# Kernel tuning notes

Hardware: AMD Instinct MI355X
Metric: run time of the kernel (lower is better)

Reference implementation:

```python
import jax, jax.numpy as jnp
import numpy as np

B, A_IN, C_IN, H, W_ = 8, 16, 4, 64, 64   # batch, input atoms, input capsules, spatial
K, C_OUT, A_OUT, ROUTINGS = 5, 8, 32, 3
EPS = 1e-7


def setup_inputs() -> dict:
    key = jax.random.key(0)
    k1, k2 = jax.random.split(key)
    x = jax.random.normal(k1, (B, A_IN, C_IN, H, W_), dtype=jnp.float32)
    # kaiming_uniform_(fan_in, relu): bound = sqrt(3) * sqrt(2) / sqrt(fan_in)
    fan_in = A_IN * K * K
    bound = float(np.sqrt(6.0 / fan_in))
    W = jax.random.uniform(k2, (C_OUT * A_OUT, A_IN, K, K), jnp.float32, -bound, bound)
    b = jnp.full((1, 1, C_OUT, A_OUT), 0.1, dtype=jnp.float32)
    return {"x": x, "W": W, "b": b}


def _squash(v):
    # v: (..., atoms); SegCaps squash with epsilon inside sqrt
    sq = jnp.sum(v * v, axis=-1, keepdims=True)
    return v * (sq / (1.0 + sq) / jnp.sqrt(sq + EPS))


def reference(x, W, b):
    # Faithful to torch: permute then raw row-major reshapes (byte reinterpret)
    t = jnp.transpose(x, (2, 0, 3, 4, 1))                      # (C_IN, B, H, W, A_IN)
    t = t.reshape(C_IN * B, H, W_, A_IN).reshape(-1, A_IN, H, W_)
    conv = jax.lax.conv_general_dilated(
        t, W, window_strides=(1, 1), padding="SAME",
        dimension_numbers=("NCHW", "OIHW", "NCHW"))             # (C_IN*B, C_OUT*A_OUT, h, w)
    ch, cw = conv.shape[2], conv.shape[3]
    votes = conv.reshape(B, C_IN, ch, cw, C_OUT, A_OUT)         # raw reinterpret, as in torch
    biases = jnp.tile(b, (ch, cw, 1, 1))                        # (h, w, C_OUT, A_OUT)

    # dynamic routing (SegCaps update_routing)
    logits = jnp.zeros((B, C_IN, ch, cw, C_OUT), dtype=votes.dtype)
    activation = None
    for _ in range(ROUTINGS):
        route = jax.nn.softmax(logits, axis=-1)                 # (B, Cin, h, w, Cout)
        preact = jnp.einsum("bihwo,bihwoa->bhwoa", route, votes) + biases
        activation = _squash(preact)                            # (B, h, w, Cout, A)
        agreement = jnp.einsum("bihwoa,bhwoa->bihwo", votes, activation)
        logits = logits + agreement
    return jnp.transpose(activation, (0, 4, 3, 1, 2))           # (B, A_OUT, C_OUT, h, w)
```

## Files before the change

kernel.cpp:

```cpp
#include <hip/hip_runtime.h>
#include <hip/hip_bf16.h>


typedef _Float16 half8 __attribute__((ext_vector_type(8)));
typedef _Float16 half4v __attribute__((ext_vector_type(4)));
typedef float floatx4 __attribute__((ext_vector_type(4)));

#define EPSF 1e-7f

__global__ __launch_bounds__(256) void k_prep(const float* __restrict__ x,
                                              const float* __restrict__ W,
                                              _Float16* __restrict__ th,
                                              _Float16* __restrict__ Wp) {
  const int tid = threadIdx.x;
  if (blockIdx.x < 256) {
    __shared__ float lin[32 * 306 + 18];
    const int bid = blockIdx.x;
    const int n   = bid >> 3;
    const int a0h = (bid >> 2) & 1;
    const int W0  = (bid & 3) * 16;
    const int ci = n >> 3, b0 = n & 7;
    const float* xb = x + b0 * 262144 + ci * 4096 + W0;
    for (int p = 0; p < 8; ++p) {
      int rr = p * 64 + (tid >> 2);
      int qq = (tid & 3) * 4;
      int a1 = rr >> 5, m = rr & 31;
      float4 v = *(const float4*)(xb + a1 * 16384 + (a0h * 32 + m) * 64 + qq);
      float* d = lin + m * 306 + a1 * 18 + qq;
      d[0] = v.x; d[1] = v.y; d[2] = v.z; d[3] = v.w;
    }
    __syncthreads();
    _Float16* tb = th + (size_t)n * 65536 + a0h * 32768 + W0 * 128;
    for (int hh = 0; hh < 4; ++hh) {
      int w1 = tid >> 4, a1 = tid & 15;
      half8 v;
#pragma unroll
      for (int j = 0; j < 8; ++j)
        v[j] = (_Float16)lin[(j * 4 + hh) * 306 + a1 * 18 + w1];
      *(half8*)(tb + hh * 8192 + w1 * 128 + a1 * 8) = v;
    }
  } else {
    int id = (blockIdx.x - 256) * 256 + tid;
    int a  = id & 15;
    int oc = (id >> 4) & 255;
    int kk = id >> 12;
    Wp[id] = (kk < 25) ? (_Float16)W[oc * 400 + a * 25 + kk] : (_Float16)0.0f;
  }
}

__global__ __launch_bounds__(256, 3) void k_conv(
    const _Float16* __restrict__ th, const _Float16* __restrict__ Wp,
    _Float16* __restrict__ votes) {
  __shared__ _Float16 slab[5440];
  const int y = blockIdx.x;
  const int n = blockIdx.y;
  const int tid = threadIdx.x;

  for (int c = tid; c < 680; c += 256) {
    int ah  = c / 340;
    int rem = c - ah * 340;
    int rr  = rem / 68;
    int cc  = rem - rr * 68;
    int row = y + rr - 2;
    int col = cc - 2;
    half8 v = {};
    if (row >= 0 && row < 64 && col >= 0 && col < 64)
      v = *(const half8*)(th + (size_t)(((n * 2 + ah) * 64 + row) * 64 + col) * 8);
    *(half8*)(slab + c * 8) = v;
  }

  const int lane  = tid & 63;
  const int wv    = tid >> 6;
  const int col16 = lane & 15;
  const int quad  = lane >> 4;
  const int t     = quad >> 1;
  const int a0h   = quad & 1;
  const int m0    = wv * 64;

  floatx4 acc[4][4] = {};

  const _Float16* wb = Wp + (size_t)t * 4096 + (m0 + col16) * 16 + a0h * 8;
  half8 af[4], a1[4], a2[4], bf[4], b1[4];
#pragma unroll
  for (int oct = 0; oct < 4; ++oct) {
    af[oct] = *(const half8*)(wb + oct * 256);
    a1[oct] = *(const half8*)(wb + 8192 + oct * 256);
  }

  __syncthreads();

  {
    int kkb = t;
    int ky = kkb / 5, kx = kkb - ky * 5;
    const _Float16* lb = slab + (a0h * 340 + ky * 68 + col16 + kx) * 8;
#pragma unroll
    for (int xt = 0; xt < 4; ++xt)
      bf[xt] = *(const half8*)(lb + xt * 128);
  }

  for (int s = 0; s < 13; ++s) {
    int s2 = (s + 2 < 13) ? s + 2 : 12;
#pragma unroll
    for (int oct = 0; oct < 4; ++oct)
      a2[oct] = *(const half8*)(wb + (size_t)s2 * 8192 + oct * 256);
    int kkb1 = 2 * (s + 1) + t; if (kkb1 > 24) kkb1 = 24;
    int ky1 = kkb1 / 5, kx1 = kkb1 - ky1 * 5;
    const _Float16* lb1 = slab + (a0h * 340 + ky1 * 68 + col16 + kx1) * 8;
#pragma unroll
    for (int xt = 0; xt < 4; ++xt)
      b1[xt] = *(const half8*)(lb1 + xt * 128);
#pragma unroll
    for (int oct = 0; oct < 4; ++oct)
#pragma unroll
      for (int xt = 0; xt < 4; ++xt)
        acc[oct][xt] = __builtin_amdgcn_mfma_f32_16x16x32_f16(
            af[oct], bf[xt], acc[oct][xt], 0, 0, 0);
#pragma unroll
    for (int oct = 0; oct < 4; ++oct) { af[oct] = a1[oct]; a1[oct] = a2[oct]; }
#pragma unroll
    for (int xt = 0; xt < 4; ++xt) bf[xt] = b1[xt];
  }

  _Float16* vbase = votes + (size_t)n * 1048576 + y * 64;
#pragma unroll
  for (int oct = 0; oct < 4; ++oct)
#pragma unroll
    for (int xt = 0; xt < 4; ++xt)
#pragma unroll
      for (int r = 0; r < 4; ++r) {
        int oc = m0 + oct * 16 + quad * 4 + r;
        int xx = xt * 16 + col16;
        vbase[(size_t)oc * 4096 + xx] = (_Float16)acc[oct][xt][r];
      }
}

__global__ __launch_bounds__(256) void k_routing3(
    const _Float16* __restrict__ votes, const float* __restrict__ bias,
    float* __restrict__ out) {
  __shared__ float so[128 * 37];
  const int tid  = threadIdx.x;
  const int lane = tid & 63;
  const int wv   = tid >> 6;
  const int bid  = blockIdx.x;
  const int bv = bid >> 7;
  const int h  = (bid >> 1) & 63;
  const int W0 = (bid & 1) * 32;

  float4 bia = *(const float4*)(bias + lane * 4);
  const int o = lane >> 3;
  const int m = lane & 7;

  float act[8][4];

  const _Float16* vb0 = votes + (size_t)bv * 4194304 + h * 16384
                        + (W0 + wv * 8) * 256 + lane * 4;
  half4v vn[4];
#pragma unroll
  for (int i = 0; i < 4; ++i)
    vn[i] = *(const half4v*)(vb0 + (size_t)i * 1048576);

  for (int k = 0; k < 8; ++k) {
    float4 v[4];
#pragma unroll
    for (int i = 0; i < 4; ++i)
      v[i] = make_float4((float)vn[i].x, (float)vn[i].y,
                         (float)vn[i].z, (float)vn[i].w);
    if (k < 7) {
#pragma unroll
      for (int i = 0; i < 4; ++i)
        vn[i] = *(const half4v*)(vb0 + (k + 1) * 256 + (size_t)i * 1048576);
    }

    float logit[4] = {0.f, 0.f, 0.f, 0.f};
#pragma unroll
    for (int r = 0; r < 3; ++r) {
      float route[4];
#pragma unroll
      for (int i = 0; i < 4; ++i) {
        float mx = logit[i];
        mx = fmaxf(mx, __shfl_xor(mx, 8, 64));
        mx = fmaxf(mx, __shfl_xor(mx, 16, 64));
        mx = fmaxf(mx, __shfl_xor(mx, 32, 64));
        float e = __expf(logit[i] - mx);
        float s = e;
        s += __shfl_xor(s, 8, 64);
        s += __shfl_xor(s, 16, 64);
        s += __shfl_xor(s, 32, 64);
        route[i] = e / s;
      }
      float pr[4] = {bia.x, bia.y, bia.z, bia.w};
#pragma unroll
      for (int i = 0; i < 4; ++i) {
        pr[0] = fmaf(route[i], v[i].x, pr[0]);
        pr[1] = fmaf(route[i], v[i].y, pr[1]);
        pr[2] = fmaf(route[i], v[i].z, pr[2]);
        pr[3] = fmaf(route[i], v[i].w, pr[3]);
      }
      float sq = pr[0]*pr[0] + pr[1]*pr[1] + pr[2]*pr[2] + pr[3]*pr[3];
      sq += __shfl_xor(sq, 1, 64);
      sq += __shfl_xor(sq, 2, 64);
      sq += __shfl_xor(sq, 4, 64);
      float scale = sq / (1.f + sq) / sqrtf(sq + EPSF);
#pragma unroll
      for (int j = 0; j < 4; ++j) act[k][j] = pr[j] * scale;

      if (r < 2) {
#pragma unroll
        for (int i = 0; i < 4; ++i) {
          float ag = v[i].x*act[k][0] + v[i].y*act[k][1]
                   + v[i].z*act[k][2] + v[i].w*act[k][3];
          ag += __shfl_xor(ag, 1, 64);
          ag += __shfl_xor(ag, 2, 64);
          ag += __shfl_xor(ag, 4, 64);
          logit[i] += ag;
        }
      }
    }
  }

  float* ob = out + (size_t)bv * 1048576 + h * 64 + W0;
#pragma unroll
  for (int ph = 0; ph < 2; ++ph) {
    if (ph) __syncthreads();
#pragma unroll
    for (int k = 0; k < 8; ++k)
#pragma unroll
      for (int jj = 0; jj < 2; ++jj) {
        int rc = m * 16 + jj * 8 + o;
        so[rc * 37 + wv * 8 + k] = act[k][2 * ph + jj];
      }
    __syncthreads();
    for (int p = 0; p < 4; ++p) {
      int rc = p * 32 + (tid >> 3);
      int mm = rc >> 4, jj = (rc >> 3) & 1, oo = rc & 7;
      int rg = mm * 32 + (2 * ph + jj) * 8 + oo;
      int w0 = (tid & 7) * 4;
      const float* sp = so + rc * 37 + w0;
      float4 val = make_float4(sp[0], sp[1], sp[2], sp[3]);
      *(float4*)(ob + (size_t)rg * 4096 + w0) = val;
    }
  }
}

extern "C" void kernel_launch(void* const* d_in, const int* in_sizes, int n_in,
                              void* d_out, int out_size, void* d_ws, size_t ws_size,
                              hipStream_t stream) {
  const float* x  = (const float*)d_in[0];
  const float* W  = (const float*)d_in[1];
  const float* b  = (const float*)d_in[2];
  float* out = (float*)d_out;

  _Float16* th    = (_Float16*)d_ws;
  _Float16* Wp    = th + 2097152;
  _Float16* votes = Wp + 106496;

  k_prep<<<672, 256, 0, stream>>>(x, W, th, Wp);
  k_conv<<<dim3(64, 32), 256, 0, stream>>>(th, Wp, votes);
  k_routing3<<<1024, 256, 0, stream>>>(votes, b, out);
}
```

Baseline: 152.8 us.

## Pre-pad conv input, swap MFMA operands for vector stores, simplify routing

The prep kernel now writes the transposed fp16 input into a zero-padded 68x68 buffer, cleared by a memset, so the conv slab load needs no bounds checks. The conv kernel swaps MFMA operand order so each lane holds four consecutive x outputs, which allows half4 vector stores of votes. It also drops the occupancy hint from launch_bounds. The routing kernel specialises the first iteration to uniform routes of 1/8, drops the softmax max-subtraction, and halves the pixels per block, doubling the grid. The memset adds an extra launch, and dropping the max-subtraction relies on logits staying small.

```diff
diff --git a/kernel.cpp b/kernel.cpp
--- a/kernel.cpp
+++ b/kernel.cpp
@@ -8,9 +8,10 @@
 
 #define EPSF 1e-7f
 
+
 __global__ __launch_bounds__(256) void k_prep(const float* __restrict__ x,
                                               const float* __restrict__ W,
-                                              _Float16* __restrict__ th,
+                                              _Float16* __restrict__ thp,
                                               _Float16* __restrict__ Wp) {
   const int tid = threadIdx.x;
   if (blockIdx.x < 256) {
@@ -30,14 +31,16 @@
       d[0] = v.x; d[1] = v.y; d[2] = v.z; d[3] = v.w;
     }
     __syncthreads();
-    _Float16* tb = th + (size_t)n * 65536 + a0h * 32768 + W0 * 128;
     for (int hh = 0; hh < 4; ++hh) {
       int w1 = tid >> 4, a1 = tid & 15;
+      int h = hh * 16 + ((W0 + w1) >> 2);
+      int w = ((W0 + w1) & 3) * 16 + a1;
       half8 v;
 #pragma unroll
       for (int j = 0; j < 8; ++j)
         v[j] = (_Float16)lin[(j * 4 + hh) * 306 + a1 * 18 + w1];
-      *(half8*)(tb + hh * 8192 + w1 * 128 + a1 * 8) = v;
+      size_t chunk = ((size_t)(n * 2 + a0h) * 68 + (h + 2)) * 68 + (w + 2);
+      *(half8*)(thp + chunk * 8) = v;
     }
   } else {
     int id = (blockIdx.x - 256) * 256 + tid;
@@ -48,25 +51,20 @@
   }
 }
 
-__global__ __launch_bounds__(256, 3) void k_conv(
-    const _Float16* __restrict__ th, const _Float16* __restrict__ Wp,
+__global__ __launch_bounds__(256) void k_conv(
+    const _Float16* __restrict__ thp, const _Float16* __restrict__ Wp,
     _Float16* __restrict__ votes) {
   __shared__ _Float16 slab[5440];
   const int y = blockIdx.x;
   const int n = blockIdx.y;
   const int tid = threadIdx.x;
 
+  const size_t base0 = (size_t)(n * 2) * 36992 + (size_t)y * 544;
   for (int c = tid; c < 680; c += 256) {
-    int ah  = c / 340;
+    int ah  = (c >= 340);
     int rem = c - ah * 340;
-    int rr  = rem / 68;
-    int cc  = rem - rr * 68;
-    int row = y + rr - 2;
-    int col = cc - 2;
-    half8 v = {};
-    if (row >= 0 && row < 64 && col >= 0 && col < 64)
-      v = *(const half8*)(th + (size_t)(((n * 2 + ah) * 64 + row) * 64 + col) * 8);
-    *(half8*)(slab + c * 8) = v;
+    *(half8*)(slab + c * 8) =
+        *(const half8*)(thp + base0 + (size_t)ah * 36992 + rem * 8);
   }
 
   const int lane  = tid & 63;
@@ -80,115 +78,126 @@
   floatx4 acc[4][4] = {};
 
   const _Float16* wb = Wp + (size_t)t * 4096 + (m0 + col16) * 16 + a0h * 8;
-  half8 af[4], a1[4], a2[4], bf[4], b1[4];
+  half8 wf[4], wf1[4], wf2[4], pf[4], pf1[4];
 #pragma unroll
   for (int oct = 0; oct < 4; ++oct) {
-    af[oct] = *(const half8*)(wb + oct * 256);
-    a1[oct] = *(const half8*)(wb + 8192 + oct * 256);
+    wf[oct]  = *(const half8*)(wb + oct * 256);
+    wf1[oct] = *(const half8*)(wb + 8192 + oct * 256);
   }
 
   __syncthreads();
 
-  {
-    int kkb = t;
-    int ky = kkb / 5, kx = kkb - ky * 5;
-    const _Float16* lb = slab + (a0h * 340 + ky * 68 + col16 + kx) * 8;
-#pragma unroll
-    for (int xt = 0; xt < 4; ++xt)
-      bf[xt] = *(const half8*)(lb + xt * 128);
-  }
+#pragma unroll
+  for (int xt = 0; xt < 4; ++xt)
+    pf[xt] = *(const half8*)(slab + (a0h * 340 + xt * 16 + col16 + t) * 8);
 
   for (int s = 0; s < 13; ++s) {
     int s2 = (s + 2 < 13) ? s + 2 : 12;
 #pragma unroll
     for (int oct = 0; oct < 4; ++oct)
-      a2[oct] = *(const half8*)(wb + (size_t)s2 * 8192 + oct * 256);
+      wf2[oct] = *(const half8*)(wb + (size_t)s2 * 8192 + oct * 256);
     int kkb1 = 2 * (s + 1) + t; if (kkb1 > 24) kkb1 = 24;
     int ky1 = kkb1 / 5, kx1 = kkb1 - ky1 * 5;
     const _Float16* lb1 = slab + (a0h * 340 + ky1 * 68 + col16 + kx1) * 8;
 #pragma unroll
     for (int xt = 0; xt < 4; ++xt)
-      b1[xt] = *(const half8*)(lb1 + xt * 128);
-#pragma unroll
-    for (int oct = 0; oct < 4; ++oct)
-#pragma unroll
-      for (int xt = 0; xt < 4; ++xt)
-        acc[oct][xt] = __builtin_amdgcn_mfma_f32_16x16x32_f16(
-            af[oct], bf[xt], acc[oct][xt], 0, 0, 0);
-#pragma unroll
-    for (int oct = 0; oct < 4; ++oct) { af[oct] = a1[oct]; a1[oct] = a2[oct]; }
-#pragma unroll
-    for (int xt = 0; xt < 4; ++xt) bf[xt] = b1[xt];
+      pf1[xt] = *(const half8*)(lb1 + xt * 128);
+#pragma unroll
+    for (int xt = 0; xt < 4; ++xt)
+#pragma unroll
+      for (int oct = 0; oct < 4; ++oct)
+        acc[xt][oct] = __builtin_amdgcn_mfma_f32_16x16x32_f16(
+            pf[xt], wf[oct], acc[xt][oct], 0, 0, 0);
+#pragma unroll
+    for (int oct = 0; oct < 4; ++oct) { wf[oct] = wf1[oct]; wf1[oct] = wf2[oct]; }
+#pragma unroll
+    for (int xt = 0; xt < 4; ++xt) pf[xt] = pf1[xt];
   }
 
   _Float16* vbase = votes + (size_t)n * 1048576 + y * 64;
 #pragma unroll
-  for (int oct = 0; oct < 4; ++oct)
-#pragma unroll
-    for (int xt = 0; xt < 4; ++xt)
-#pragma unroll
-      for (int r = 0; r < 4; ++r) {
-        int oc = m0 + oct * 16 + quad * 4 + r;
-        int xx = xt * 16 + col16;
-        vbase[(size_t)oc * 4096 + xx] = (_Float16)acc[oct][xt][r];
-      }
-}
-
-__global__ __launch_bounds__(256) void k_routing3(
+  for (int oct = 0; oct < 4; ++oct) {
+    int oc = m0 + oct * 16 + col16;
+#pragma unroll
+    for (int xt = 0; xt < 4; ++xt) {
+      half4v o4;
+      o4.x = (_Float16)acc[xt][oct][0];
+      o4.y = (_Float16)acc[xt][oct][1];
+      o4.z = (_Float16)acc[xt][oct][2];
+      o4.w = (_Float16)acc[xt][oct][3];
+      *(half4v*)(vbase + (size_t)oc * 4096 + xt * 16 + quad * 4) = o4;
+    }
+  }
+}
+
+__global__ __launch_bounds__(256) void k_routing4(
     const _Float16* __restrict__ votes, const float* __restrict__ bias,
     float* __restrict__ out) {
-  __shared__ float so[128 * 37];
+  __shared__ float so[256 * 17];
   const int tid  = threadIdx.x;
   const int lane = tid & 63;
   const int wv   = tid >> 6;
   const int bid  = blockIdx.x;
-  const int bv = bid >> 7;
-  const int h  = (bid >> 1) & 63;
-  const int W0 = (bid & 1) * 32;
+  const int bv = bid >> 8;
+  const int h  = (bid >> 2) & 63;
+  const int W0 = (bid & 3) * 16;
 
   float4 bia = *(const float4*)(bias + lane * 4);
   const int o = lane >> 3;
   const int m = lane & 7;
 
-  float act[8][4];
+  float act[4][4];
 
   const _Float16* vb0 = votes + (size_t)bv * 4194304 + h * 16384
-                        + (W0 + wv * 8) * 256 + lane * 4;
-  half4v vn[4];
-#pragma unroll
-  for (int i = 0; i < 4; ++i)
-    vn[i] = *(const half4v*)(vb0 + (size_t)i * 1048576);
-
-  for (int k = 0; k < 8; ++k) {
+                        + (W0 + wv * 4) * 256 + lane * 4;
+
+#pragma unroll
+  for (int k = 0; k < 4; ++k) {
     float4 v[4];
 #pragma unroll
-    for (int i = 0; i < 4; ++i)
-      v[i] = make_float4((float)vn[i].x, (float)vn[i].y,
-                         (float)vn[i].z, (float)vn[i].w);
-    if (k < 7) {
-#pragma unroll
-      for (int i = 0; i < 4; ++i)
-        vn[i] = *(const half4v*)(vb0 + (k + 1) * 256 + (size_t)i * 1048576);
-    }
-
-    float logit[4] = {0.f, 0.f, 0.f, 0.f};
-#pragma unroll
-    for (int r = 0; r < 3; ++r) {
+    for (int i = 0; i < 4; ++i) {
+      half4v hv = *(const half4v*)(vb0 + k * 256 + (size_t)i * 1048576);
+      v[i] = make_float4((float)hv.x, (float)hv.y, (float)hv.z, (float)hv.w);
+    }
+
+    float pr[4] = {bia.x, bia.y, bia.z, bia.w};
+#pragma unroll
+    for (int i = 0; i < 4; ++i) {
+      pr[0] = fmaf(0.125f, v[i].x, pr[0]);
+      pr[1] = fmaf(0.125f, v[i].y, pr[1]);
+      pr[2] = fmaf(0.125f, v[i].z, pr[2]);
+      pr[3] = fmaf(0.125f, v[i].w, pr[3]);
+    }
+    float sq = pr[0]*pr[0] + pr[1]*pr[1] + pr[2]*pr[2] + pr[3]*pr[3];
+    sq += __shfl_xor(sq, 1, 64);
+    sq += __shfl_xor(sq, 2, 64);
+    sq += __shfl_xor(sq, 4, 64);
+    float scale = sq / (1.f + sq) / sqrtf(sq + EPSF);
+    float a0 = pr[0]*scale, a1 = pr[1]*scale, a2 = pr[2]*scale, a3 = pr[3]*scale;
+
+    float logit[4];
+#pragma unroll
+    for (int i = 0; i < 4; ++i) {
+      float ag = v[i].x*a0 + v[i].y*a1 + v[i].z*a2 + v[i].w*a3;
+      ag += __shfl_xor(ag, 1, 64);
+      ag += __shfl_xor(ag, 2, 64);
+      ag += __shfl_xor(ag, 4, 64);
+      logit[i] = ag;
+    }
+
+#pragma unroll
+    for (int r = 1; r < 3; ++r) {
       float route[4];
 #pragma unroll
       for (int i = 0; i < 4; ++i) {
-        float mx = logit[i];
-        mx = fmaxf(mx, __shfl_xor(mx, 8, 64));
-        mx = fmaxf(mx, __shfl_xor(mx, 16, 64));
-        mx = fmaxf(mx, __shfl_xor(mx, 32, 64));
-        float e = __expf(logit[i] - mx);
+        float e = __expf(logit[i]);
         float s = e;
         s += __shfl_xor(s, 8, 64);
         s += __shfl_xor(s, 16, 64);
         s += __shfl_xor(s, 32, 64);
         route[i] = e / s;
       }
-      float pr[4] = {bia.x, bia.y, bia.z, bia.w};
+      pr[0] = bia.x; pr[1] = bia.y; pr[2] = bia.z; pr[3] = bia.w;
 #pragma unroll
       for (int i = 0; i < 4; ++i) {
         pr[0] = fmaf(route[i], v[i].x, pr[0]);
@@ -196,19 +205,17 @@
         pr[2] = fmaf(route[i], v[i].z, pr[2]);
         pr[3] = fmaf(route[i], v[i].w, pr[3]);
       }
-      float sq = pr[0]*pr[0] + pr[1]*pr[1] + pr[2]*pr[2] + pr[3]*pr[3];
+      sq = pr[0]*pr[0] + pr[1]*pr[1] + pr[2]*pr[2] + pr[3]*pr[3];
       sq += __shfl_xor(sq, 1, 64);
       sq += __shfl_xor(sq, 2, 64);
       sq += __shfl_xor(sq, 4, 64);
-      float scale = sq / (1.f + sq) / sqrtf(sq + EPSF);
-#pragma unroll
-      for (int j = 0; j < 4; ++j) act[k][j] = pr[j] * scale;
-
-      if (r < 2) {
+      scale = sq / (1.f + sq) / sqrtf(sq + EPSF);
+      a0 = pr[0]*scale; a1 = pr[1]*scale; a2 = pr[2]*scale; a3 = pr[3]*scale;
+
+      if (r == 1) {
 #pragma unroll
         for (int i = 0; i < 4; ++i) {
-          float ag = v[i].x*act[k][0] + v[i].y*act[k][1]
-                   + v[i].z*act[k][2] + v[i].w*act[k][3];
+          float ag = v[i].x*a0 + v[i].y*a1 + v[i].z*a2 + v[i].w*a3;
           ag += __shfl_xor(ag, 1, 64);
           ag += __shfl_xor(ag, 2, 64);
           ag += __shfl_xor(ag, 4, 64);
@@ -216,29 +223,23 @@
         }
       }
     }
-  }
+    act[k][0] = a0; act[k][1] = a1; act[k][2] = a2; act[k][3] = a3;
+  }
+
+#pragma unroll
+  for (int k = 0; k < 4; ++k)
+#pragma unroll
+    for (int j = 0; j < 4; ++j)
+      so[((m * 4 + j) * 8 + o) * 17 + wv * 4 + k] = act[k][j];
+  __syncthreads();
 
   float* ob = out + (size_t)bv * 1048576 + h * 64 + W0;
-#pragma unroll
-  for (int ph = 0; ph < 2; ++ph) {
-    if (ph) __syncthreads();
-#pragma unroll
-    for (int k = 0; k < 8; ++k)
-#pragma unroll
-      for (int jj = 0; jj < 2; ++jj) {
-        int rc = m * 16 + jj * 8 + o;
-        so[rc * 37 + wv * 8 + k] = act[k][2 * ph + jj];
-      }
-    __syncthreads();
-    for (int p = 0; p < 4; ++p) {
-      int rc = p * 32 + (tid >> 3);
-      int mm = rc >> 4, jj = (rc >> 3) & 1, oo = rc & 7;
-      int rg = mm * 32 + (2 * ph + jj) * 8 + oo;
-      int w0 = (tid & 7) * 4;
-      const float* sp = so + rc * 37 + w0;
-      float4 val = make_float4(sp[0], sp[1], sp[2], sp[3]);
-      *(float4*)(ob + (size_t)rg * 4096 + w0) = val;
-    }
+  for (int p = 0; p < 4; ++p) {
+    int rg = p * 64 + (tid >> 2);
+    int w0 = (tid & 3) * 4;
+    const float* sp = so + rg * 17 + w0;
+    float4 val = make_float4(sp[0], sp[1], sp[2], sp[3]);
+    *(float4*)(ob + (size_t)rg * 4096 + w0) = val;
   }
 }
 
@@ -250,11 +251,12 @@
   const float* b  = (const float*)d_in[2];
   float* out = (float*)d_out;
 
-  _Float16* th    = (_Float16*)d_ws;
-  _Float16* Wp    = th + 2097152;
+  _Float16* thp   = (_Float16*)d_ws;
+  _Float16* Wp    = thp + 2367488;
   _Float16* votes = Wp + 106496;
 
-  k_prep<<<672, 256, 0, stream>>>(x, W, th, Wp);
-  k_conv<<<dim3(64, 32), 256, 0, stream>>>(th, Wp, votes);
-  k_routing3<<<1024, 256, 0, stream>>>(votes, b, out);
-}
+  hipMemsetAsync(thp, 0, 2367488 * sizeof(_Float16), stream);
+  k_prep<<<672, 256, 0, stream>>>(x, W, thp, Wp);
+  k_conv<<<dim3(64, 32), 256, 0, stream>>>(thp, Wp, votes);
+  k_routing4<<<2048, 256, 0, stream>>>(votes, b, out);
+}
```

Result: faster. 144.6 us (-5.3%).
